# Kernel tuning notes

Measured on AMD Instinct MI355X. Metric: run time of the kernel, lower is better.

The kernel has to match this reference:

```python
import jax, jax.numpy as jnp
import numpy as np
from jax import lax


def setup_inputs() -> dict:
    key = jax.random.key(0)
    k1, k2 = jax.random.split(key)
    B, N, C, H, W = 4, 32, 32, 64, 64
    x = jax.random.normal(k1, (B, N, C, H, W), dtype=jnp.float32)
    # grouped conv weight: groups = N*C, 1 input channel per group, 3 outputs per group
    w = jax.random.normal(k2, (3 * N * C, 1, 1, 1), dtype=jnp.float32) * 0.1
    return {"x": x, "w": w}


def reference(x, w):
    B, N, C, H, W = x.shape
    xc = x.reshape(B, N * C, H, W)
    # grouped 1x1 conv (groups = N*C), matches nn.Conv2d(inC*N, 3*qkvC*N, 1, groups=qkvC*N, bias=False)
    qkv = lax.conv_general_dilated(
        xc, w,
        window_strides=(1, 1), padding=[(0, 0), (0, 0)],
        feature_group_count=N * C,
        dimension_numbers=("NCHW", "OIHW", "NCHW"),
    )
    qkv = qkv.reshape(B, N, C, 3, H, W)
    scale = (H * W) ** (-0.5)
    q = scale * qkv[:, :, :, 0]           # (B,N,C,H,W)
    k = qkv[:, :, :, 1]
    v = qkv[:, :, :, 2]
    # original: 6D einsum (a,b,c,d,e,f) then sum over d,e == contraction over H,W
    S = jnp.einsum("bachw,bfchw->bcaf", q, k)   # (B,C,N,N)
    A = jax.nn.softmax(S, axis=-1)
    # original: broadcast-multiply with v and sum over f
    out = jnp.einsum("bcaf,bfchw->abchw", A, v)  # (N,B,C,H,W)
    return out
```

## Files before the change

### kernel.cpp

```cpp
#include <hip/hip_runtime.h>

typedef __attribute__((ext_vector_type(8))) short bf16x8;
typedef __attribute__((ext_vector_type(4))) float f32x4;

#define BB 4
#define NN 32
#define CC 32
#define HWD 4096
#define AROW ((size_t)CC * HWD)

__device__ __forceinline__ unsigned cvt_pk_bf16(float lo, float hi) {
    unsigned r;
    asm("v_cvt_pk_bf16_f32 %0, %1, %2" : "=v"(r) : "v"(lo), "v"(hi));
    return r;
}

__device__ __forceinline__ bf16x8 pack8(float4 a, float4 b) {
    union { unsigned u[4]; bf16x8 v; } u;
    u.u[0] = cvt_pk_bf16(a.x, a.y);
    u.u[1] = cvt_pk_bf16(a.z, a.w);
    u.u[2] = cvt_pk_bf16(b.x, b.y);
    u.u[3] = cvt_pk_bf16(b.z, b.w);
    return u.v;
}

__global__ __launch_bounds__(256) void k_gram(const float* __restrict__ x,
                                              float* __restrict__ Gp) {
    const int bid = blockIdx.x;
    const int s   = bid & 7;
    const int bc  = bid >> 3;
    const int b   = bc >> 5, c = bc & 31;
    const int tid = threadIdx.x;
    const int w   = tid >> 6, l = tid & 63;
    const int r   = l & 15, g = l >> 4;

    const float* xb = x + ((size_t)b * NN * CC + c) * HWD;
    const int hwbase = s * 512 + w * 128;
    const float* p0 = xb + (size_t)r        * AROW + hwbase + 8 * g;
    const float* p1 = xb + (size_t)(r + 16) * AROW + hwbase + 8 * g;

    f32x4 acc[2][2];
#pragma unroll
    for (int i = 0; i < 2; ++i)
#pragma unroll
        for (int j = 0; j < 2; ++j)
#pragma unroll
            for (int q = 0; q < 4; ++q) acc[i][j][q] = 0.f;

#pragma unroll
    for (int ch = 0; ch < 4; ++ch) {
        const float4 a0 = *(const float4*)(p0 + ch * 32);
        const float4 a1 = *(const float4*)(p0 + ch * 32 + 4);
        const float4 b0 = *(const float4*)(p1 + ch * 32);
        const float4 b1 = *(const float4*)(p1 + ch * 32 + 4);
        const bf16x8 F0 = pack8(a0, a1);
        const bf16x8 F1 = pack8(b0, b1);
        acc[0][0] = __builtin_amdgcn_mfma_f32_16x16x32_bf16(F0, F0, acc[0][0], 0, 0, 0);
        acc[0][1] = __builtin_amdgcn_mfma_f32_16x16x32_bf16(F0, F1, acc[0][1], 0, 0, 0);
        acc[1][0] = __builtin_amdgcn_mfma_f32_16x16x32_bf16(F1, F0, acc[1][0], 0, 0, 0);
        acc[1][1] = __builtin_amdgcn_mfma_f32_16x16x32_bf16(F1, F1, acc[1][1], 0, 0, 0);
    }

    __shared__ float red[4][64][16];
#pragma unroll
    for (int ta = 0; ta < 2; ++ta)
#pragma unroll
        for (int tf = 0; tf < 2; ++tf)
#pragma unroll
            for (int q = 0; q < 4; ++q)
                red[w][l][(ta * 2 + tf) * 4 + q] = acc[ta][tf][q];
    __syncthreads();

    const int a   = tid >> 3;
    const int f0  = 4 * (tid & 7);
    const int lg  = ((a >> 2) & 3) * 16 + (f0 & 15);
    const int reg = ((a >> 4) * 2 + (f0 >> 4)) * 4 + (a & 3);
    float sv[4];
#pragma unroll
    for (int j = 0; j < 4; ++j) {
        float v = 0.f;
#pragma unroll
        for (int ww = 0; ww < 4; ++ww) v += red[ww][lg + j][reg];
        sv[j] = v;
    }
    *(float4*)&Gp[(size_t)bid * 1024 + 4 * tid] = make_float4(sv[0], sv[1], sv[2], sv[3]);
}

__global__ __launch_bounds__(256) void k_softmax(const float* __restrict__ Gp,
                                                 const float* __restrict__ w,
                                                 unsigned short* __restrict__ Ahat) {
    const int bc = blockIdx.x;
    const int c  = bc & 31;
    const int t  = threadIdx.x;
    const int a  = t >> 3, fo = 4 * (t & 7);

    float gs[4] = {0.f, 0.f, 0.f, 0.f};
#pragma unroll
    for (int s = 0; s < 8; ++s) {
        const float4 v = *(const float4*)&Gp[(size_t)(bc * 8 + s) * 1024 + a * 32 + fo];
        gs[0] += v.x; gs[1] += v.y; gs[2] += v.z; gs[3] += v.w;
    }
    const float wq = w[(a * CC + c) * 3] * 0.015625f;
    float S[4];
#pragma unroll
    for (int j = 0; j < 4; ++j)
        S[j] = wq * w[((fo + j) * CC + c) * 3 + 1] * gs[j];

    float m = fmaxf(fmaxf(S[0], S[1]), fmaxf(S[2], S[3]));
#pragma unroll
    for (int o = 1; o < 8; o <<= 1) m = fmaxf(m, __shfl_xor(m, o, 64));
    float e[4], sum = 0.f;
#pragma unroll
    for (int j = 0; j < 4; ++j) { e[j] = __expf(S[j] - m); sum += e[j]; }
#pragma unroll
    for (int o = 1; o < 8; o <<= 1) sum += __shfl_xor(sum, o, 64);
    const float inv = 1.f / sum;

    float o0 = e[0] * inv * w[((fo + 0) * CC + c) * 3 + 2];
    float o1 = e[1] * inv * w[((fo + 1) * CC + c) * 3 + 2];
    float o2 = e[2] * inv * w[((fo + 2) * CC + c) * 3 + 2];
    float o3 = e[3] * inv * w[((fo + 3) * CC + c) * 3 + 2];
    uint2 pk = make_uint2(cvt_pk_bf16(o0, o1), cvt_pk_bf16(o2, o3));
    *(uint2*)&Ahat[(size_t)bc * 1024 + a * 32 + fo] = pk;
}

__global__ __launch_bounds__(256) void k_pv(const float* __restrict__ x,
                                            const unsigned short* __restrict__ Ahat,
                                            float* __restrict__ out) {
    const int bid   = blockIdx.x;
    const int chunk = bid & 15;
    const int bc    = bid >> 4;
    const int b     = bc >> 5, c = bc & 31;
    const int tid   = threadIdx.x;
    const int w     = tid >> 6, l = tid & 63;
    const int r     = l & 15, g = l >> 4;

    const unsigned short* ab = Ahat + (size_t)bc * 1024;
    const bf16x8 A0 = *(const bf16x8*)(ab + r * 32 + 8 * g);
    const bf16x8 A1 = *(const bf16x8*)(ab + (r + 16) * 32 + 8 * g);

    const float* xb = x + ((size_t)b * NN * CC + c) * HWD + chunk * 256 + w * 64;
    const f32x4 zero = {0.f, 0.f, 0.f, 0.f};

#pragma unroll
    for (int ht = 0; ht < 4; ++ht) {
        const int hw = ht * 16 + r;
        const float* bp = xb + (size_t)(8 * g) * AROW + hw;
        float bf[8];
#pragma unroll
        for (int i = 0; i < 8; ++i) bf[i] = bp[(size_t)i * AROW];
        const bf16x8 B = pack8(make_float4(bf[0], bf[1], bf[2], bf[3]),
                               make_float4(bf[4], bf[5], bf[6], bf[7]));
        f32x4 d0 = __builtin_amdgcn_mfma_f32_16x16x32_bf16(A0, B, zero, 0, 0, 0);
        f32x4 d1 = __builtin_amdgcn_mfma_f32_16x16x32_bf16(A1, B, zero, 0, 0, 0);

        const size_t hwg = (size_t)chunk * 256 + w * 64 + ht * 16 + r;
#pragma unroll
        for (int q = 0; q < 4; ++q) {
            const int arow0 = g * 4 + q;
            out[(((size_t)arow0 * BB + b) * CC + c) * HWD + hwg]        = d0[q];
            out[(((size_t)(arow0 + 16) * BB + b) * CC + c) * HWD + hwg] = d1[q];
        }
    }
}

extern "C" void kernel_launch(void* const* d_in, const int* in_sizes, int n_in,
                              void* d_out, int out_size, void* d_ws, size_t ws_size,
                              hipStream_t stream) {
    const float* x = (const float*)d_in[0];
    const float* w = (const float*)d_in[1];
    float* outp = (float*)d_out;
    float* Gp = (float*)d_ws;
    unsigned short* Ahat = (unsigned short*)((char*)d_ws + (size_t)4 * 1024 * 1024);

    hipLaunchKernelGGL(k_gram,    dim3(1024), dim3(256), 0, stream, x, Gp);
    hipLaunchKernelGGL(k_softmax, dim3(128),  dim3(256), 0, stream, Gp, w, Ahat);
    hipLaunchKernelGGL(k_pv,      dim3(2048), dim3(256), 0, stream, x, Ahat, outp);
}
```

Before: 44.18 us.

## Fuse softmax into PV kernel and stage x tile through swizzled LDS

Removes the separate softmax launch: every PV block now recomputes the softmax for its (b,c) from the partial Gram sums and keeps the bf16 attention weights in shared memory. The x tile is loaded with coalesced float4 reads, packed to bf16 and transposed into a swizzled LDS buffer, replacing strided scalar global loads. The cost is redundant softmax work, 16 times per (b,c), plus extra Gp reads, LDS use and a barrier per block.

Result: slower. 45.81 us (+3.7%).

```diff
diff --git a/kernel.cpp b/kernel.cpp
--- a/kernel.cpp
+++ b/kernel.cpp
@@ -86,80 +86,91 @@
     *(float4*)&Gp[(size_t)bid * 1024 + 4 * tid] = make_float4(sv[0], sv[1], sv[2], sv[3]);
 }
 
-__global__ __launch_bounds__(256) void k_softmax(const float* __restrict__ Gp,
-                                                 const float* __restrict__ w,
-                                                 unsigned short* __restrict__ Ahat) {
-    const int bc = blockIdx.x;
-    const int c  = bc & 31;
-    const int t  = threadIdx.x;
-    const int a  = t >> 3, fo = 4 * (t & 7);
-
-    float gs[4] = {0.f, 0.f, 0.f, 0.f};
-#pragma unroll
-    for (int s = 0; s < 8; ++s) {
-        const float4 v = *(const float4*)&Gp[(size_t)(bc * 8 + s) * 1024 + a * 32 + fo];
-        gs[0] += v.x; gs[1] += v.y; gs[2] += v.z; gs[3] += v.w;
-    }
-    const float wq = w[(a * CC + c) * 3] * 0.015625f;
-    float S[4];
-#pragma unroll
-    for (int j = 0; j < 4; ++j)
-        S[j] = wq * w[((fo + j) * CC + c) * 3 + 1] * gs[j];
-
-    float m = fmaxf(fmaxf(S[0], S[1]), fmaxf(S[2], S[3]));
-#pragma unroll
-    for (int o = 1; o < 8; o <<= 1) m = fmaxf(m, __shfl_xor(m, o, 64));
-    float e[4], sum = 0.f;
-#pragma unroll
-    for (int j = 0; j < 4; ++j) { e[j] = __expf(S[j] - m); sum += e[j]; }
-#pragma unroll
-    for (int o = 1; o < 8; o <<= 1) sum += __shfl_xor(sum, o, 64);
-    const float inv = 1.f / sum;
-
-    float o0 = e[0] * inv * w[((fo + 0) * CC + c) * 3 + 2];
-    float o1 = e[1] * inv * w[((fo + 1) * CC + c) * 3 + 2];
-    float o2 = e[2] * inv * w[((fo + 2) * CC + c) * 3 + 2];
-    float o3 = e[3] * inv * w[((fo + 3) * CC + c) * 3 + 2];
-    uint2 pk = make_uint2(cvt_pk_bf16(o0, o1), cvt_pk_bf16(o2, o3));
-    *(uint2*)&Ahat[(size_t)bc * 1024 + a * 32 + fo] = pk;
-}
-
 __global__ __launch_bounds__(256) void k_pv(const float* __restrict__ x,
-                                            const unsigned short* __restrict__ Ahat,
+                                            const float* __restrict__ w,
+                                            const float* __restrict__ Gp,
                                             float* __restrict__ out) {
     const int bid   = blockIdx.x;
     const int chunk = bid & 15;
     const int bc    = bid >> 4;
     const int b     = bc >> 5, c = bc & 31;
     const int tid   = threadIdx.x;
-    const int w     = tid >> 6, l = tid & 63;
+    const int wv    = tid >> 6, l = tid & 63;
     const int r     = l & 15, g = l >> 4;
 
-    const unsigned short* ab = Ahat + (size_t)bc * 1024;
-    const bf16x8 A0 = *(const bf16x8*)(ab + r * 32 + 8 * g);
-    const bf16x8 A1 = *(const bf16x8*)(ab + (r + 16) * 32 + 8 * g);
+    __shared__ unsigned xt[256][16];
+    __shared__ unsigned ahat[32][20];
 
-    const float* xb = x + ((size_t)b * NN * CC + c) * HWD + chunk * 256 + w * 64;
+    {
+        const int a = tid >> 3, fo = 4 * (tid & 7);
+        float gs[4] = {0.f, 0.f, 0.f, 0.f};
+#pragma unroll
+        for (int s = 0; s < 8; ++s) {
+            const float4 v = *(const float4*)&Gp[(size_t)(bc * 8 + s) * 1024 + a * 32 + fo];
+            gs[0] += v.x; gs[1] += v.y; gs[2] += v.z; gs[3] += v.w;
+        }
+        const float wq = w[(a * CC + c) * 3] * 0.015625f;
+        float S[4];
+#pragma unroll
+        for (int j = 0; j < 4; ++j)
+            S[j] = wq * w[((fo + j) * CC + c) * 3 + 1] * gs[j];
+
+        float m = fmaxf(fmaxf(S[0], S[1]), fmaxf(S[2], S[3]));
+#pragma unroll
+        for (int o = 1; o < 8; o <<= 1) m = fmaxf(m, __shfl_xor(m, o, 64));
+        float e[4], sum = 0.f;
+#pragma unroll
+        for (int j = 0; j < 4; ++j) { e[j] = __expf(S[j] - m); sum += e[j]; }
+#pragma unroll
+        for (int o = 1; o < 8; o <<= 1) sum += __shfl_xor(sum, o, 64);
+        const float inv = 1.f / sum;
+
+        const float o0 = e[0] * inv * w[((fo + 0) * CC + c) * 3 + 2];
+        const float o1 = e[1] * inv * w[((fo + 1) * CC + c) * 3 + 2];
+        const float o2 = e[2] * inv * w[((fo + 2) * CC + c) * 3 + 2];
+        const float o3 = e[3] * inv * w[((fo + 3) * CC + c) * 3 + 2];
+        ahat[a][2 * (tid & 7) + 0] = cvt_pk_bf16(o0, o1);
+        ahat[a][2 * (tid & 7) + 1] = cvt_pk_bf16(o2, o3);
+    }
+
+    {
+        const int p = tid >> 4;
+        const int q = tid & 15;
+        const float* xr0 = x + ((size_t)(b * NN + 2 * p) * CC + c) * HWD + chunk * 256;
+        const float* xr1 = xr0 + AROW;
+#pragma unroll
+        for (int k = 0; k < 4; ++k) {
+            const int hwc = 4 * (q + 16 * k);
+            const float4 fa = *(const float4*)(xr0 + hwc);
+            const float4 fb = *(const float4*)(xr1 + hwc);
+            const float av[4] = {fa.x, fa.y, fa.z, fa.w};
+            const float bv[4] = {fb.x, fb.y, fb.z, fb.w};
+#pragma unroll
+            for (int i = 0; i < 4; ++i) {
+                const int hw = hwc + i;
+                xt[hw][p ^ (hw & 12)] = cvt_pk_bf16(av[i], bv[i]);
+            }
+        }
+    }
+    __syncthreads();
+
+    const bf16x8 A0 = *(const bf16x8*)&ahat[r][4 * g];
+    const bf16x8 A1 = *(const bf16x8*)&ahat[r + 16][4 * g];
     const f32x4 zero = {0.f, 0.f, 0.f, 0.f};
 
 #pragma unroll
     for (int ht = 0; ht < 4; ++ht) {
-        const int hw = ht * 16 + r;
-        const float* bp = xb + (size_t)(8 * g) * AROW + hw;
-        float bf[8];
-#pragma unroll
-        for (int i = 0; i < 8; ++i) bf[i] = bp[(size_t)i * AROW];
-        const bf16x8 B = pack8(make_float4(bf[0], bf[1], bf[2], bf[3]),
-                               make_float4(bf[4], bf[5], bf[6], bf[7]));
+        const int hw = wv * 64 + ht * 16 + r;
+        const bf16x8 B = *(const bf16x8*)&xt[hw][4 * (g ^ ((hw >> 2) & 3))];
         f32x4 d0 = __builtin_amdgcn_mfma_f32_16x16x32_bf16(A0, B, zero, 0, 0, 0);
         f32x4 d1 = __builtin_amdgcn_mfma_f32_16x16x32_bf16(A1, B, zero, 0, 0, 0);
 
-        const size_t hwg = (size_t)chunk * 256 + w * 64 + ht * 16 + r;
+        const size_t hwg = (size_t)chunk * 256 + hw;
 #pragma unroll
-        for (int q = 0; q < 4; ++q) {
-            const int arow0 = g * 4 + q;
-            out[(((size_t)arow0 * BB + b) * CC + c) * HWD + hwg]        = d0[q];
-            out[(((size_t)(arow0 + 16) * BB + b) * CC + c) * HWD + hwg] = d1[q];
+        for (int q2 = 0; q2 < 4; ++q2) {
+            const int a0r = g * 4 + q2;
+            out[(((size_t)a0r * BB + b) * CC + c) * HWD + hwg]        = d0[q2];
+            out[(((size_t)(a0r + 16) * BB + b) * CC + c) * HWD + hwg] = d1[q2];
         }
     }
 }
@@ -171,9 +182,7 @@
     const float* w = (const float*)d_in[1];
     float* outp = (float*)d_out;
     float* Gp = (float*)d_ws;
-    unsigned short* Ahat = (unsigned short*)((char*)d_ws + (size_t)4 * 1024 * 1024);
 
-    hipLaunchKernelGGL(k_gram,    dim3(1024), dim3(256), 0, stream, x, Gp);
-    hipLaunchKernelGGL(k_softmax, dim3(128),  dim3(256), 0, stream, Gp, w, Ahat);
-    hipLaunchKernelGGL(k_pv,      dim3(2048), dim3(256), 0, stream, x, Ahat, outp);
+    hipLaunchKernelGGL(k_gram, dim3(1024), dim3(256), 0, stream, x, Gp);
+    hipLaunchKernelGGL(k_pv,   dim3(2048), dim3(256), 0, stream, x, w, Gp, outp);
 }
```
